# Kernel optimization log

Measured on AMD Instinct MI355X. Metric: run time of the kernel, lower is better.

## Reference

```python
import jax, jax.numpy as jnp
import numpy as np

N = 100000      # nodes
E = 1600000     # edges (avg degree 16)
DIN = 3         # input_dim (xyz coords)
DOUT = 64       # output_dim
EPS = 1e-5      # LayerNorm eps


def setup_inputs() -> dict:
    key = jax.random.key(0)
    ks = jax.random.split(key, 6)
    x = jax.random.normal(ks[0], (N, DIN), jnp.float32)
    edge_index = jax.random.randint(ks[1], (2, E), 0, N, dtype=jnp.int64)
    # li1: Linear(DIN, DOUT)
    W1 = jax.random.normal(ks[2], (DIN, DOUT), jnp.float32) / np.sqrt(DIN)
    b1 = jnp.zeros((DOUT,), jnp.float32)
    # gcn1: GCNConv(DOUT, DOUT) -> weight + bias
    Wg = jax.random.normal(ks[3], (DOUT, DOUT), jnp.float32) / np.sqrt(DOUT)
    bg = jnp.zeros((DOUT,), jnp.float32)
    # norm1d: LayerNorm(2*DOUT)
    gamma = jnp.ones((2 * DOUT,), jnp.float32)
    beta = jnp.zeros((2 * DOUT,), jnp.float32)
    return {"x": x, "edge_index": edge_index, "W1": W1, "b1": b1,
            "Wg": Wg, "bg": bg, "gamma": gamma, "beta": beta}


def reference(x, edge_index, W1, b1, Wg, bg, gamma, beta):
    n = x.shape[0]
    # li1 + act
    h = jax.nn.relu(x @ W1 + b1)                       # [N, DOUT]
    # GCNConv: add self loops, symmetric normalization D^-1/2 (A+I) D^-1/2
    loops = jnp.arange(n, dtype=edge_index.dtype)
    src = jnp.concatenate([edge_index[0], loops])      # [E+N]
    dst = jnp.concatenate([edge_index[1], loops])      # [E+N]
    deg = jax.ops.segment_sum(jnp.ones_like(dst, h.dtype), dst, num_segments=n)
    dinv = jnp.where(deg > 0, jax.lax.rsqrt(jnp.maximum(deg, 1.0)), 0.0)
    norm = dinv[src] * dinv[dst]                       # [E+N]
    hg = h @ Wg                                        # [N, DOUT]
    agg = jax.ops.segment_sum(hg[src] * norm[:, None], dst, num_segments=n)
    h2 = jax.nn.relu(agg + bg)                         # [N, DOUT]
    # concat + LayerNorm(2*DOUT)
    cat = jnp.concatenate([h, h2], axis=1)             # [N, 2*DOUT]
    mu = jnp.mean(cat, axis=-1, keepdims=True)
    var = jnp.mean(jnp.square(cat - mu), axis=-1, keepdims=True)
    return (cat - mu) * jax.lax.rsqrt(var + EPS) * gamma + beta
```

## Files before the change

kernel.cpp:

```cpp
#include <hip/hip_runtime.h>
#include <math.h>

#define N_NODES 100000
#define N_EDGES 1600000
#define EPS_    1e-5f
#define PAD     64
#define SCOL    48


#define NCHUNK_E 782
#define EPB_E    2048
#define NB_EDGE  (NCHUNK_E * 8)
#define PART_SZ  12500

#define LIN_WAVES 1563

typedef float v16f __attribute__((ext_vector_type(16)));

__device__ __forceinline__ float bf2f(unsigned short u) {
    union { unsigned int i; float f; } v; v.i = (unsigned int)u << 16; return v.f;
}
__device__ __forceinline__ unsigned short f2bf(float f) {
    union { float f; unsigned int i; } v; v.f = f;
    unsigned int b = v.i + 0x7FFFu + ((v.i >> 16) & 1u);
    return (unsigned short)(b >> 16);
}
__device__ __forceinline__ unsigned int pk2(float lo, float hi) {
    return (unsigned int)f2bf(lo) | ((unsigned int)f2bf(hi) << 16);
}

#define FMA16(A, wv0, wv1, wv2, wv3)                                          \
    do {                                                                      \
        A[0]  = fmaf(hk, wv0.x, A[0]);  A[1]  = fmaf(hk, wv0.y, A[1]);        \
        A[2]  = fmaf(hk, wv0.z, A[2]);  A[3]  = fmaf(hk, wv0.w, A[3]);        \
        A[4]  = fmaf(hk, wv1.x, A[4]);  A[5]  = fmaf(hk, wv1.y, A[5]);        \
        A[6]  = fmaf(hk, wv1.z, A[6]);  A[7]  = fmaf(hk, wv1.w, A[7]);        \
        A[8]  = fmaf(hk, wv2.x, A[8]);  A[9]  = fmaf(hk, wv2.y, A[9]);        \
        A[10] = fmaf(hk, wv2.z, A[10]); A[11] = fmaf(hk, wv2.w, A[11]);       \
        A[12] = fmaf(hk, wv3.x, A[12]); A[13] = fmaf(hk, wv3.y, A[13]);       \
        A[14] = fmaf(hk, wv3.z, A[14]); A[15] = fmaf(hk, wv3.w, A[15]);       \
    } while (0)

__global__ void fused_edge_lin_kernel(const int* __restrict__ src,
                                      const int* __restrict__ dst,
                                      const float* __restrict__ x,
                                      const float* __restrict__ W1,
                                      const float* __restrict__ b1,
                                      const float* __restrict__ Wg,
                                      int* __restrict__ cnt,
                                      int* __restrict__ ell,
                                      unsigned short* __restrict__ hb_g)
{
    const int tl    = threadIdx.x;
    const int part  = blockIdx.x & 7;
    const int chunk = blockIdx.x >> 3;
    const int lo    = part * PART_SZ;
    const int hi    = lo + PART_SZ;

    const int ebase = chunk * EPB_E + tl * 8;
    int dv[8], sv[8], pos[8];
    if (ebase + 8 <= N_EDGES) {
        const int4 d0 = *(const int4*)(dst + ebase);
        const int4 d1 = *(const int4*)(dst + ebase + 4);
        const int4 s0 = *(const int4*)(src + ebase);
        const int4 s1 = *(const int4*)(src + ebase + 4);
        dv[0] = d0.x; dv[1] = d0.y; dv[2] = d0.z; dv[3] = d0.w;
        dv[4] = d1.x; dv[5] = d1.y; dv[6] = d1.z; dv[7] = d1.w;
        sv[0] = s0.x; sv[1] = s0.y; sv[2] = s0.z; sv[3] = s0.w;
        sv[4] = s1.x; sv[5] = s1.y; sv[6] = s1.z; sv[7] = s1.w;
    } else {
#pragma unroll
        for (int j = 0; j < 8; ++j) {
            const int e = ebase + j;
            if (e < N_EDGES) { dv[j] = dst[e]; sv[j] = src[e]; }
            else             { dv[j] = -1;     sv[j] = 0;      }
        }
    }
#pragma unroll
    for (int j = 0; j < 8; ++j) {
        pos[j] = -1;
        if (dv[j] >= lo && dv[j] < hi) pos[j] = atomicAdd(&cnt[dv[j]], 1);
    }

    const int wave = blockIdx.x * 4 + (tl >> 6);
    if (wave < LIN_WAVES) {
        const int lane = tl & 63;
        const int n    = wave * 64 + lane;
        const bool act = (n < N_NODES);
        float x0 = 0.f, x1 = 0.f, x2 = 0.f;
        if (act) { x0 = x[n * 3]; x1 = x[n * 3 + 1]; x2 = x[n * 3 + 2]; }

        v16f a0, a1, a2, a3;
#pragma unroll
        for (int i = 0; i < 16; ++i) { a0[i] = 0.f; a1[i] = 0.f; a2[i] = 0.f; a3[i] = 0.f; }

        for (int k = 0; k < 64; ++k) {
            const float w0 = W1[k];
            const float w1 = W1[64 + k];
            const float w2 = W1[128 + k];
            const float bb = b1[k];
            const float hk = fmaxf(fmaf(x0, w0, fmaf(x1, w1, fmaf(x2, w2, bb))), 0.f);

            const float4* __restrict__ r4 = (const float4*)(Wg + (size_t)k * 64);
            {
                const float4 p0 = r4[0], p1 = r4[1], p2 = r4[2], p3 = r4[3];
                FMA16(a0, p0, p1, p2, p3);
            }
            {
                const float4 p0 = r4[4], p1 = r4[5], p2 = r4[6], p3 = r4[7];
                FMA16(a1, p0, p1, p2, p3);
            }
            {
                const float4 p0 = r4[8], p1 = r4[9], p2 = r4[10], p3 = r4[11];
                FMA16(a2, p0, p1, p2, p3);
            }
            {
                const float4 p0 = r4[12], p1 = r4[13], p2 = r4[14], p3 = r4[15];
                FMA16(a3, p0, p1, p2, p3);
            }
        }

        if (act) {
            uint4* __restrict__ dp = (uint4*)(hb_g + (size_t)n * 64);
            dp[0] = make_uint4(pk2(a0[0],  a0[1]),  pk2(a0[2],  a0[3]),
                               pk2(a0[4],  a0[5]),  pk2(a0[6],  a0[7]));
            dp[1] = make_uint4(pk2(a0[8],  a0[9]),  pk2(a0[10], a0[11]),
                               pk2(a0[12], a0[13]), pk2(a0[14], a0[15]));
            dp[2] = make_uint4(pk2(a1[0],  a1[1]),  pk2(a1[2],  a1[3]),
                               pk2(a1[4],  a1[5]),  pk2(a1[6],  a1[7]));
            dp[3] = make_uint4(pk2(a1[8],  a1[9]),  pk2(a1[10], a1[11]),
                               pk2(a1[12], a1[13]), pk2(a1[14], a1[15]));
            dp[4] = make_uint4(pk2(a2[0],  a2[1]),  pk2(a2[2],  a2[3]),
                               pk2(a2[4],  a2[5]),  pk2(a2[6],  a2[7]));
            dp[5] = make_uint4(pk2(a2[8],  a2[9]),  pk2(a2[10], a2[11]),
                               pk2(a2[12], a2[13]), pk2(a2[14], a2[15]));
            dp[6] = make_uint4(pk2(a3[0],  a3[1]),  pk2(a3[2],  a3[3]),
                               pk2(a3[4],  a3[5]),  pk2(a3[6],  a3[7]));
            dp[7] = make_uint4(pk2(a3[8],  a3[9]),  pk2(a3[10], a3[11]),
                               pk2(a3[12], a3[13]), pk2(a3[14], a3[15]));
        }
    }

#pragma unroll
    for (int j = 0; j < 8; ++j)
        if (pos[j] >= 0 && pos[j] < PAD) ell[dv[j] * PAD + pos[j]] = sv[j];
}

__global__ void scale_kernel(const int* __restrict__ cnt,
                             unsigned int* __restrict__ g2)
{
    const int t = blockIdx.x * blockDim.x + threadIdx.x;
    if (t >= N_NODES * 32) return;
    const int node = t >> 5;
    const float di = rsqrtf((float)(cnt[node] + 1));
    const unsigned int v = g2[t];
    const float lo = bf2f((unsigned short)(v & 0xFFFFu)) * di;
    const float hi = bf2f((unsigned short)(v >> 16)) * di;
    g2[t] = (unsigned int)f2bf(lo) | ((unsigned int)f2bf(hi) << 16);
}

__global__ void gather_final_kernel(const unsigned short* __restrict__ hb_g,
                                    const int* __restrict__ cnt,
                                    const int* __restrict__ ell,
                                    const float* __restrict__ x,
                                    const float* __restrict__ W1,
                                    const float* __restrict__ b1,
                                    const float* __restrict__ bg,
                                    const float* __restrict__ gamma,
                                    const float* __restrict__ beta,
                                    float* __restrict__ out)
{
    __shared__ int sell[64 * SCOL];
    __shared__ int lcnt[64];
    const int tl = threadIdx.x;
    const int b  = blockIdx.x;
    const int nb = b * 64;

    if (tl < 64) {
        const int n = nb + tl;
        lcnt[tl] = (n < N_NODES) ? cnt[n] : 0;
    }
    {
        const int r = tl >> 2;
        const int q = tl & 3;
        const int nr = nb + r;
        if (nr < N_NODES) {
            const int4* __restrict__ grow = (const int4*)(ell + (size_t)nr * PAD);
            int4* __restrict__ srow = (int4*)(sell + r * SCOL);
            srow[q]     = grow[q];
            srow[q + 4] = grow[q + 4];
            srow[q + 8] = grow[q + 8];
        }
    }
    __syncthreads();

    const int lane = tl & 63;
    const int w    = tl >> 6;
    const float w0 = W1[lane], w1 = W1[64 + lane], w2 = W1[128 + lane];
    const float bb1 = b1[lane];
    const float bgl = bg[lane];
    const float g0 = gamma[lane], g1 = gamma[64 + lane];
    const float be0 = beta[lane], be1 = beta[64 + lane];

    for (int nl = w; nl < 64; nl += 4) {
        const int n = nb + nl;
        if (n >= N_NODES) break;

        const int c    = lcnt[nl];
        const float di = rsqrtf((float)(c + 1));
        const int deg  = (c < PAD) ? c : PAD;
        const int dstg = (deg < SCOL) ? deg : SCOL;
        const int* row = sell + nl * SCOL;

        const float xx0 = x[n * 3], xx1 = x[n * 3 + 1], xx2 = x[n * 3 + 2];
        float acc = bf2f(hb_g[(size_t)n * 64 + lane]);

        int j = 0;
        for (; j + 8 <= dstg; j += 8) {
            const int4 r0 = *(const int4*)(row + j);
            const int4 r1 = *(const int4*)(row + j + 4);
            const float a0 = bf2f(hb_g[(size_t)r0.x * 64 + lane]);
            const float a1 = bf2f(hb_g[(size_t)r0.y * 64 + lane]);
            const float a2 = bf2f(hb_g[(size_t)r0.z * 64 + lane]);
            const float a3 = bf2f(hb_g[(size_t)r0.w * 64 + lane]);
            const float a4 = bf2f(hb_g[(size_t)r1.x * 64 + lane]);
            const float a5 = bf2f(hb_g[(size_t)r1.y * 64 + lane]);
            const float a6 = bf2f(hb_g[(size_t)r1.z * 64 + lane]);
            const float a7 = bf2f(hb_g[(size_t)r1.w * 64 + lane]);
            acc += ((a0 + a1) + (a2 + a3)) + ((a4 + a5) + (a6 + a7));
        }
        if (j + 4 <= dstg) {
            const int4 r0 = *(const int4*)(row + j);
            acc += (bf2f(hb_g[(size_t)r0.x * 64 + lane]) + bf2f(hb_g[(size_t)r0.y * 64 + lane]))
                 + (bf2f(hb_g[(size_t)r0.z * 64 + lane]) + bf2f(hb_g[(size_t)r0.w * 64 + lane]));
            j += 4;
        }
        for (; j < dstg; ++j) acc += bf2f(hb_g[(size_t)row[j] * 64 + lane]);
        for (; j < deg; ++j)
            acc += bf2f(hb_g[(size_t)ell[(size_t)n * PAD + j] * 64 + lane]);

        float h  = fmaxf(fmaf(xx0, w0, fmaf(xx1, w1, fmaf(xx2, w2, bb1))), 0.f);
        float h2 = fmaxf(fmaf(di, acc, bgl), 0.f);

        float sum = h + h2;
#pragma unroll
        for (int o = 32; o > 0; o >>= 1) sum += __shfl_xor(sum, o, 64);
        const float mu = sum * (1.0f / 128.0f);

        const float dA = h  - mu;
        const float dB = h2 - mu;
        float vs = dA * dA + dB * dB;
#pragma unroll
        for (int o = 32; o > 0; o >>= 1) vs += __shfl_xor(vs, o, 64);
        const float rr = rsqrtf(vs * (1.0f / 128.0f) + EPS_);

        out[(size_t)n * 128 + lane]      = dA * rr * g0 + be0;
        out[(size_t)n * 128 + 64 + lane] = dB * rr * g1 + be1;
    }
}

extern "C" void kernel_launch(void* const* d_in, const int* in_sizes, int n_in,
                              void* d_out, int out_size, void* d_ws, size_t ws_size,
                              hipStream_t stream)
{
    const float* x     = (const float*)d_in[0];
    const int*   edge  = (const int*)  d_in[1];
    const float* W1    = (const float*)d_in[2];
    const float* b1    = (const float*)d_in[3];
    const float* Wg    = (const float*)d_in[4];
    const float* bg    = (const float*)d_in[5];
    const float* gamma = (const float*)d_in[6];
    const float* beta  = (const float*)d_in[7];
    float*       out   = (float*)d_out;

    char*  ws  = (char*)d_ws;
    size_t p   = 0;
    unsigned short* hb_g = (unsigned short*)(ws + p); p += (size_t)N_NODES * 64 * sizeof(unsigned short);
    int*            ell  = (int*)           (ws + p); p += (size_t)N_NODES * PAD * sizeof(int);
    int*            cnt  = (int*)           (ws + p);

    const int* src = edge;
    const int* dst = edge + N_EDGES;

    hipMemsetAsync(cnt, 0, (size_t)N_NODES * sizeof(int), stream);

    fused_edge_lin_kernel<<<NB_EDGE, 256, 0, stream>>>(src, dst, x, W1, b1, Wg,
                                                       cnt, ell, hb_g);
    scale_kernel<<<(N_NODES * 32 + 255) / 256, 256, 0, stream>>>(cnt, (unsigned int*)hb_g);
    gather_final_kernel<<<(N_NODES + 63) / 64, 256, 0, stream>>>(hb_g, cnt, ell,
                                                                 x, W1, b1,
                                                                 bg, gamma, beta, out);
}
```

Before: 215.2 us.

## Gather two neighbor rows per wave using packed bf16x2 half-wave loads

```diff
diff --git a/kernel.cpp b/kernel.cpp
--- a/kernel.cpp
+++ b/kernel.cpp
@@ -15,6 +15,9 @@
 
 #define LIN_WAVES 1563
 
+#define GF_NODES 32
+#define NB_GATHER ((N_NODES + GF_NODES - 1) / GF_NODES)
+
 typedef float v16f __attribute__((ext_vector_type(16)));
 
 __device__ __forceinline__ float bf2f(unsigned short u) {
@@ -27,6 +30,12 @@
 }
 __device__ __forceinline__ unsigned int pk2(float lo, float hi) {
     return (unsigned int)f2bf(lo) | ((unsigned int)f2bf(hi) << 16);
+}
+__device__ __forceinline__ float u2lo(unsigned int v) {
+    union { unsigned int i; float f; } u; u.i = v << 16; return u.f;
+}
+__device__ __forceinline__ float u2hi(unsigned int v) {
+    union { unsigned int i; float f; } u; u.i = v & 0xFFFF0000u; return u.f;
 }
 
 #define FMA16(A, wv0, wv1, wv2, wv3)                                          \
@@ -170,13 +179,13 @@
                                     const float* __restrict__ beta,
                                     float* __restrict__ out)
 {
-    __shared__ int sell[64 * SCOL];
-    __shared__ int lcnt[64];
+    __shared__ int sell[GF_NODES * SCOL];
+    __shared__ int lcnt[GF_NODES];
     const int tl = threadIdx.x;
     const int b  = blockIdx.x;
-    const int nb = b * 64;
-
-    if (tl < 64) {
+    const int nb = b * GF_NODES;
+
+    if (tl < GF_NODES) {
         const int n = nb + tl;
         lcnt[tl] = (n < N_NODES) ? cnt[n] : 0;
     }
@@ -196,13 +205,17 @@
 
     const int lane = tl & 63;
     const int w    = tl >> 6;
+    const int half = lane >> 5;
+    const int l32  = lane & 31;
+    const int off  = 1 - half;
+
     const float w0 = W1[lane], w1 = W1[64 + lane], w2 = W1[128 + lane];
     const float bb1 = b1[lane];
     const float bgl = bg[lane];
     const float g0 = gamma[lane], g1 = gamma[64 + lane];
     const float be0 = beta[lane], be1 = beta[64 + lane];
 
-    for (int nl = w; nl < 64; nl += 4) {
+    for (int nl = w; nl < GF_NODES; nl += 2) {
         const int n = nb + nl;
         if (n >= N_NODES) break;
 
@@ -213,31 +226,64 @@
         const int* row = sell + nl * SCOL;
 
         const float xx0 = x[n * 3], xx1 = x[n * 3 + 1], xx2 = x[n * 3 + 2];
-        float acc = bf2f(hb_g[(size_t)n * 64 + lane]);
-
-        int j = 0;
-        for (; j + 8 <= dstg; j += 8) {
-            const int4 r0 = *(const int4*)(row + j);
-            const int4 r1 = *(const int4*)(row + j + 4);
-            const float a0 = bf2f(hb_g[(size_t)r0.x * 64 + lane]);
-            const float a1 = bf2f(hb_g[(size_t)r0.y * 64 + lane]);
-            const float a2 = bf2f(hb_g[(size_t)r0.z * 64 + lane]);
-            const float a3 = bf2f(hb_g[(size_t)r0.w * 64 + lane]);
-            const float a4 = bf2f(hb_g[(size_t)r1.x * 64 + lane]);
-            const float a5 = bf2f(hb_g[(size_t)r1.y * 64 + lane]);
-            const float a6 = bf2f(hb_g[(size_t)r1.z * 64 + lane]);
-            const float a7 = bf2f(hb_g[(size_t)r1.w * 64 + lane]);
-            acc += ((a0 + a1) + (a2 + a3)) + ((a4 + a5) + (a6 + a7));
-        }
-        if (j + 4 <= dstg) {
-            const int4 r0 = *(const int4*)(row + j);
-            acc += (bf2f(hb_g[(size_t)r0.x * 64 + lane]) + bf2f(hb_g[(size_t)r0.y * 64 + lane]))
-                 + (bf2f(hb_g[(size_t)r0.z * 64 + lane]) + bf2f(hb_g[(size_t)r0.w * 64 + lane]));
-            j += 4;
-        }
-        for (; j < dstg; ++j) acc += bf2f(hb_g[(size_t)row[j] * 64 + lane]);
-        for (; j < deg; ++j)
-            acc += bf2f(hb_g[(size_t)ell[(size_t)n * PAD + j] * 64 + lane]);
+
+        float acc0 = 0.f, acc1 = 0.f;
+        if (half == 0) {
+            const unsigned int v = *(const unsigned int*)(hb_g + (size_t)n * 64 + l32 * 2);
+            acc0 += u2lo(v); acc1 += u2hi(v);
+        }
+
+        int bj = 0;
+        for (; bj + 16 <= dstg; bj += 16) {
+            const int i0 = row[bj + 0  + off];
+            const int i1 = row[bj + 2  + off];
+            const int i2 = row[bj + 4  + off];
+            const int i3 = row[bj + 6  + off];
+            const int i4 = row[bj + 8  + off];
+            const int i5 = row[bj + 10 + off];
+            const int i6 = row[bj + 12 + off];
+            const int i7 = row[bj + 14 + off];
+            const unsigned int v0 = *(const unsigned int*)(hb_g + (size_t)i0 * 64 + l32 * 2);
+            const unsigned int v1 = *(const unsigned int*)(hb_g + (size_t)i1 * 64 + l32 * 2);
+            const unsigned int v2 = *(const unsigned int*)(hb_g + (size_t)i2 * 64 + l32 * 2);
+            const unsigned int v3 = *(const unsigned int*)(hb_g + (size_t)i3 * 64 + l32 * 2);
+            const unsigned int v4 = *(const unsigned int*)(hb_g + (size_t)i4 * 64 + l32 * 2);
+            const unsigned int v5 = *(const unsigned int*)(hb_g + (size_t)i5 * 64 + l32 * 2);
+            const unsigned int v6 = *(const unsigned int*)(hb_g + (size_t)i6 * 64 + l32 * 2);
+            const unsigned int v7 = *(const unsigned int*)(hb_g + (size_t)i7 * 64 + l32 * 2);
+            acc0 += ((u2lo(v0) + u2lo(v1)) + (u2lo(v2) + u2lo(v3)))
+                  + ((u2lo(v4) + u2lo(v5)) + (u2lo(v6) + u2lo(v7)));
+            acc1 += ((u2hi(v0) + u2hi(v1)) + (u2hi(v2) + u2hi(v3)))
+                  + ((u2hi(v4) + u2hi(v5)) + (u2hi(v6) + u2hi(v7)));
+        }
+        if (bj + 8 <= dstg) {
+            const int i0 = row[bj + 0 + off];
+            const int i1 = row[bj + 2 + off];
+            const int i2 = row[bj + 4 + off];
+            const int i3 = row[bj + 6 + off];
+            const unsigned int v0 = *(const unsigned int*)(hb_g + (size_t)i0 * 64 + l32 * 2);
+            const unsigned int v1 = *(const unsigned int*)(hb_g + (size_t)i1 * 64 + l32 * 2);
+            const unsigned int v2 = *(const unsigned int*)(hb_g + (size_t)i2 * 64 + l32 * 2);
+            const unsigned int v3 = *(const unsigned int*)(hb_g + (size_t)i3 * 64 + l32 * 2);
+            acc0 += (u2lo(v0) + u2lo(v1)) + (u2lo(v2) + u2lo(v3));
+            acc1 += (u2hi(v0) + u2hi(v1)) + (u2hi(v2) + u2hi(v3));
+            bj += 8;
+        }
+        for (; bj < deg; bj += 2) {
+            const int my = bj + off;
+            if (my < deg) {
+                const int s = (my < dstg) ? row[my] : ell[(size_t)n * PAD + my];
+                const unsigned int v = *(const unsigned int*)(hb_g + (size_t)s * 64 + l32 * 2);
+                acc0 += u2lo(v); acc1 += u2hi(v);
+            }
+        }
+
+        acc0 += __shfl_xor(acc0, 32, 64);
+        acc1 += __shfl_xor(acc1, 32, 64);
+        const int p = lane >> 1;
+        const float e0 = __shfl(acc0, p, 64);
+        const float e1 = __shfl(acc1, p, 64);
+        const float acc = (lane & 1) ? e1 : e0;
 
         float h  = fmaxf(fmaf(xx0, w0, fmaf(xx1, w1, fmaf(xx2, w2, bb1))), 0.f);
         float h2 = fmaxf(fmaf(di, acc, bgl), 0.f);
@@ -287,7 +333,7 @@
     fused_edge_lin_kernel<<<NB_EDGE, 256, 0, stream>>>(src, dst, x, W1, b1, Wg,
                                                        cnt, ell, hb_g);
     scale_kernel<<<(N_NODES * 32 + 255) / 256, 256, 0, stream>>>(cnt, (unsigned int*)hb_g);
-    gather_final_kernel<<<(N_NODES + 63) / 64, 256, 0, stream>>>(hb_g, cnt, ell,
-                                                                 x, W1, b1,
-                                                                 bg, gamma, beta, out);
-}
+    gather_final_kernel<<<NB_GATHER, 128, 0, stream>>>(hb_g, cnt, ell,
+                                                       x, W1, b1,
+                                                       bg, gamma, beta, out);
+}
```

After: 217.6 us. No clear change (+1.1%).
